# Performance work log

Measured on AMD Instinct MI355X. Metric: run time of the kernel, lower is better.

The kernel has to match this reference:

```python
import jax, jax.numpy as jnp
import numpy as np

LN_EPS = 1e-5

def _layernorm(x, g, b):
    m = jnp.mean(x, axis=-1, keepdims=True)
    v = jnp.var(x, axis=-1, keepdims=True)
    return (x - m) / jnp.sqrt(v + LN_EPS) * g + b

def setup_inputs() -> dict:
    key = jax.random.key(0)
    ks = jax.random.split(key, 16)
    N, E, D, P = 25000, 500000, 256, 64  # nodes, edges, node_dim, pair_dim
    def rn(k, shape, scale=1.0):
        return jax.random.normal(k, shape, dtype=jnp.float32) * scale
    return {
        "x": rn(ks[0], (N, D)),
        "rbf_r": rn(ks[1], (E, P)),
        "factor_r": jax.random.uniform(ks[2], (E, 1), dtype=jnp.float32),
        "sph_v0": rn(ks[3], (E, 5, 1)),  # l=2 spherical harmonics (5 comps)
        "sph_v1": rn(ks[4], (E, 3, 1)),  # l=1 spherical harmonics (3 comps)
        "W_down": rn(ks[5], (D, P), D ** -0.5),
        "b_down": jnp.zeros((P,), jnp.float32),
        "W_up0": rn(ks[6], (P, 2 * P), P ** -0.5),
        "b_up0": jnp.zeros((2 * P,), jnp.float32),
        "W_up1": rn(ks[7], (P, 2 * P), P ** -0.5),
        "W_uph": rn(ks[8], (P, 2 * P), P ** -0.5),
        "W_n1": rn(ks[9], (6 * P, D), (6 * P) ** -0.5),
        "b_n1": jnp.zeros((D,), jnp.float32),
        "ln_g": jnp.ones((D,), jnp.float32),
        "ln_b": jnp.zeros((D,), jnp.float32),
        "W_n2": rn(ks[10], (D, D), D ** -0.5),
        "b_n2": jnp.zeros((D,), jnp.float32),
        "j": jax.random.randint(ks[11], (E,), 0, N, dtype=jnp.int32),
        "i": jax.random.randint(ks[12], (E,), 0, N, dtype=jnp.int32),
    }

def reference(x, rbf_r, factor_r, sph_v0, sph_v1, W_down, b_down, W_up0, b_up0,
              W_up1, W_uph, W_n1, b_n1, ln_g, ln_b, W_n2, b_n2, j, i):
    N = x.shape[0]
    _x = x @ W_down + b_down                      # [N, P]
    l0_pair = _x[j] * rbf_r * factor_r            # [E, P]
    agg0 = jax.ops.segment_sum(l0_pair, i, num_segments=N)                     # [N, P]
    agg1 = jax.ops.segment_sum(l0_pair[:, None, :] * sph_v1, i, num_segments=N)  # [N, 3, P]
    aggh = jax.ops.segment_sum(l0_pair[:, None, :] * sph_v0, i, num_segments=N)  # [N, 5, P]
    l0_node = (_x * agg0) @ W_up0 + b_up0                                      # [N, 2P]
    l1_node = jnp.sum(jnp.square((_x[:, None, :] * agg1) @ W_up1), axis=1)     # [N, 2P]
    lh_node = jnp.sum(jnp.square((_x[:, None, :] * aggh) @ W_uph), axis=1)     # [N, 2P]
    node = jnp.concatenate([l0_node, l1_node, lh_node], axis=-1)               # [N, 6P]
    h = jax.nn.silu(_layernorm(node @ W_n1 + b_n1, ln_g, ln_b))
    return h @ W_n2 + b_n2 + x  # dropout is identity in eval
```

## Files before the change

### kernel.cpp

```cpp
#include <hip/hip_runtime.h>
#include <hip/hip_bf16.h>

typedef __attribute__((ext_vector_type(8))) short bf16x8;
typedef __attribute__((ext_vector_type(4))) float f32x4;

__device__ __forceinline__ unsigned short f2bf(float f) {
    unsigned u = __float_as_uint(f);
    return (unsigned short)((u + 0x7FFF + ((u >> 16) & 1)) >> 16);
}
__device__ __forceinline__ unsigned pack2(float a, float b) {
    return (unsigned)f2bf(a) | ((unsigned)f2bf(b) << 16);
}
__device__ __forceinline__ float ubf(unsigned short h) {
    return __uint_as_float((unsigned)h << 16);
}
__device__ __forceinline__ int RLi(float v, int k) {
    return __builtin_amdgcn_readlane(__float_as_int(v), k);
}
__device__ __forceinline__ float RLf(float v, int k) {
    return __uint_as_float((unsigned)__builtin_amdgcn_readlane(__float_as_int(v), k));
}

__device__ void swz_body(const float* __restrict__ W,
                         unsigned short* __restrict__ Bsw, int K, int idx)
{
    int total = (K >> 5) * 1024;
    if (idx >= total) return;
    int lane = idx & 63;
    int ct = (idx >> 6) & 15;
    int ks = idx >> 10;
    int col = ct * 16 + (lane & 15);
    int kbase = (ks << 5) + ((lane >> 4) << 3);
    const float* p = &W[(size_t)kbase * 256 + col];
    uint4 o;
    o.x = pack2(p[0 * 256], p[1 * 256]);
    o.y = pack2(p[2 * 256], p[3 * 256]);
    o.z = pack2(p[4 * 256], p[5 * 256]);
    o.w = pack2(p[6 * 256], p[7 * 256]);
    *(uint4*)&Bsw[(size_t)idx * 8] = o;
}

__device__ void swz_split_body(const float* __restrict__ W,
                               unsigned short* __restrict__ Bh,
                               unsigned short* __restrict__ Bl,
                               int K, int C, int idx)
{
    int ct_n = C >> 4;
    int total = (K >> 5) * ct_n * 64;
    if (idx >= total) return;
    int per_ks = ct_n * 64;
    int ks = idx / per_ks;
    int rem = idx - ks * per_ks;
    int ct = rem >> 6;
    int lane = rem & 63;
    int col = ct * 16 + (lane & 15);
    int kbase = (ks << 5) + ((lane >> 4) << 3);
    const float* p = &W[(size_t)kbase * C + col];
    unsigned short hs[8], ls[8];
#pragma unroll
    for (int j = 0; j < 8; j++) {
        float wv = p[(size_t)j * C];
        unsigned short h = f2bf(wv);
        hs[j] = h;
        ls[j] = f2bf(wv - ubf(h));
    }
    uint4 oh, ol;
    oh.x = (unsigned)hs[0] | ((unsigned)hs[1] << 16);
    oh.y = (unsigned)hs[2] | ((unsigned)hs[3] << 16);
    oh.z = (unsigned)hs[4] | ((unsigned)hs[5] << 16);
    oh.w = (unsigned)hs[6] | ((unsigned)hs[7] << 16);
    ol.x = (unsigned)ls[0] | ((unsigned)ls[1] << 16);
    ol.y = (unsigned)ls[2] | ((unsigned)ls[3] << 16);
    ol.z = (unsigned)ls[4] | ((unsigned)ls[5] << 16);
    ol.w = (unsigned)ls[6] | ((unsigned)ls[7] << 16);
    *(uint4*)&Bh[(size_t)idx * 8] = oh;
    *(uint4*)&Bl[(size_t)idx * 8] = ol;
}

__global__ __launch_bounds__(256) void k_prep(
    const float* __restrict__ Wn1, unsigned short* __restrict__ Bsw1,
    const float* __restrict__ Wn2, unsigned short* __restrict__ Bsw2,
    const float* __restrict__ Wu0, unsigned short* __restrict__ Wu0h, unsigned short* __restrict__ Wu0l,
    const float* __restrict__ Wu1, unsigned short* __restrict__ Wu1h, unsigned short* __restrict__ Wu1l,
    const float* __restrict__ Wuh, unsigned short* __restrict__ Wuhh, unsigned short* __restrict__ Wuhl,
    const float* __restrict__ Wd, unsigned short* __restrict__ Wdh, unsigned short* __restrict__ Wdl,
    int* __restrict__ counts, int N)
{
    int b = blockIdx.x;
    int tid = threadIdx.x;
    if (b < 48)       swz_body(Wn1, Bsw1, 384, b * 256 + tid);
    else if (b < 80)  swz_body(Wn2, Bsw2, 256, (b - 48) * 256 + tid);
    else if (b < 84)  swz_split_body(Wu0, Wu0h, Wu0l, 64, 128, (b - 80) * 256 + tid);
    else if (b < 88)  swz_split_body(Wu1, Wu1h, Wu1l, 64, 128, (b - 84) * 256 + tid);
    else if (b < 92)  swz_split_body(Wuh, Wuhh, Wuhl, 64, 128, (b - 88) * 256 + tid);
    else if (b < 100) swz_split_body(Wd, Wdh, Wdl, 256, 64, (b - 92) * 256 + tid);
    else {
        for (int i = (b - 100) * 256 + tid; i < N + 1; i += 25 * 256)
            counts[i] = 0;
    }
}

__global__ __launch_bounds__(256, 4) void k_down_hist(
    const float* __restrict__ x, const unsigned short* __restrict__ Wdh,
    const unsigned short* __restrict__ Wdl, const float* __restrict__ bd,
    float* __restrict__ xp, const int* __restrict__ iidx,
    int* __restrict__ counts, int N, int E, int nDown)
{
    __shared__ __align__(16) unsigned short Ahi[32 * 264];
    __shared__ __align__(16) unsigned short Alo[32 * 264];

    if ((int)blockIdx.x >= nDown) {
        int e = ((int)blockIdx.x - nDown) * 256 + threadIdx.x;
        if (e < E) atomicAdd(&counts[iidx[e]], 1);
        return;
    }

    int n0 = blockIdx.x * 32;
    int tid = threadIdx.x;
    int lane = tid & 63;
    int w = tid >> 6;
    int rt = w & 1;
    int cg = w >> 1;
    int lcol = lane & 15;
    int quad = lane >> 4;
    int kq = quad * 8;

    for (int t = tid; t < 32 * 64; t += 256) {
        int r = t >> 6, c4 = t & 63;
        int n = n0 + r;
        float4 v = {0.f, 0.f, 0.f, 0.f};
        if (n < N) v = *(const float4*)&x[(size_t)n * 256 + c4 * 4];
        unsigned short hx = f2bf(v.x), hy = f2bf(v.y);
        unsigned short hz = f2bf(v.z), hw = f2bf(v.w);
        uint2 oh, ol;
        oh.x = (unsigned)hx | ((unsigned)hy << 16);
        oh.y = (unsigned)hz | ((unsigned)hw << 16);
        ol.x = (unsigned)f2bf(v.x - ubf(hx)) | ((unsigned)f2bf(v.y - ubf(hy)) << 16);
        ol.y = (unsigned)f2bf(v.z - ubf(hz)) | ((unsigned)f2bf(v.w - ubf(hw)) << 16);
        *(uint2*)&Ahi[r * 264 + c4 * 4] = oh;
        *(uint2*)&Alo[r * 264 + c4 * 4] = ol;
    }
    __syncthreads();

    int arow = rt * 16 + lcol;
    f32x4 acc[2];
    acc[0] = (f32x4){0.f, 0.f, 0.f, 0.f};
    acc[1] = (f32x4){0.f, 0.f, 0.f, 0.f};
#pragma unroll
    for (int ks = 0; ks < 8; ks++) {
        bf16x8 ah = *(const bf16x8*)&Ahi[arow * 264 + ks * 32 + kq];
        bf16x8 al = *(const bf16x8*)&Alo[arow * 264 + ks * 32 + kq];
#pragma unroll
        for (int t = 0; t < 2; t++) {
            int ct = cg * 2 + t;
            size_t bi = ((size_t)((ks * 4 + ct) * 64 + lane)) * 8;
            bf16x8 bh = *(const bf16x8*)&Wdh[bi];
            bf16x8 bl = *(const bf16x8*)&Wdl[bi];
            acc[t] = __builtin_amdgcn_mfma_f32_16x16x32_bf16(ah, bh, acc[t], 0, 0, 0);
            acc[t] = __builtin_amdgcn_mfma_f32_16x16x32_bf16(ah, bl, acc[t], 0, 0, 0);
            acc[t] = __builtin_amdgcn_mfma_f32_16x16x32_bf16(al, bh, acc[t], 0, 0, 0);
        }
    }
#pragma unroll
    for (int t = 0; t < 2; t++) {
        int col = cg * 32 + t * 16 + lcol;
        float bb = bd[col];
#pragma unroll
        for (int q = 0; q < 4; q++) {
            int row = rt * 16 + quad * 4 + q;
            int n = n0 + row;
            if (n < N) xp[(size_t)n * 64 + col] = acc[t][q] + bb;
        }
    }
}

__global__ __launch_bounds__(1024) void k_scan(
    const int* __restrict__ counts, int* __restrict__ rowptr,
    int* __restrict__ cursor, int N)
{
    __shared__ int part[1024];
    int t = threadIdx.x;
    int chunk = (N + 1023) / 1024;
    int beg = t * chunk;
    int end = min(beg + chunk, N);
    int s = 0;
    for (int i = beg; i < end; i++) s += counts[i];
    part[t] = s;
    __syncthreads();
    for (int off = 1; off < 1024; off <<= 1) {
        int v = (t >= off) ? part[t - off] : 0;
        __syncthreads();
        part[t] += v;
        __syncthreads();
    }
    int run = (t == 0) ? 0 : part[t - 1];
    for (int i = beg; i < end; i++) {
        rowptr[i] = run;
        cursor[i] = run;
        run += counts[i];
    }
    if (t == 1023) rowptr[N] = part[1023];
}

__global__ __launch_bounds__(256) void k_scatter_pack(
    const int* __restrict__ iidx, const int* __restrict__ jidx,
    const float* __restrict__ factor, const float* __restrict__ sph0,
    const float* __restrict__ sph1, int* __restrict__ cursor,
    float* __restrict__ packed, int E)
{
    int e = blockIdx.x * 256 + threadIdx.x;
    if (e >= E) return;
    int pos = atomicAdd(&cursor[iidx[e]], 1);
    float4 w0, w1, w2;
    w0.x = __int_as_float(e);
    w0.y = __int_as_float(jidx[e]);
    w0.z = factor[e];
    w0.w = sph1[e * 3 + 0];
    w1.x = sph1[e * 3 + 1];
    w1.y = sph1[e * 3 + 2];
    w1.z = sph0[e * 5 + 0];
    w1.w = sph0[e * 5 + 1];
    w2.x = sph0[e * 5 + 2];
    w2.y = sph0[e * 5 + 3];
    w2.z = sph0[e * 5 + 4];
    w2.w = 0.f;
    float4* q = (float4*)&packed[(size_t)pos * 12];
    q[0] = w0; q[1] = w1; q[2] = w2;
}

__global__ __launch_bounds__(256) void k_gather(
    const float* __restrict__ xp, const float* __restrict__ rbf,
    const float* __restrict__ packed, const int* __restrict__ rowptr,
    unsigned short* __restrict__ aggHi, unsigned short* __restrict__ aggLo,
    int N)
{
    int n = blockIdx.x * 4 + (threadIdx.x >> 6);
    if (n >= N) return;
    int p = threadIdx.x & 63;
    int beg = rowptr[n], end = rowptr[n + 1];

    float a0 = 0.f;
    float a1x = 0.f, a1y = 0.f, a1z = 0.f;
    float h0 = 0.f, h1 = 0.f, h2 = 0.f, h3 = 0.f, h4 = 0.f;

    for (int base = beg; base < end; base += 64) {
        int m = end - base;
        if (m > 64) m = 64;
        float4 w0 = {0.f, 0.f, 0.f, 0.f};
        float4 w1 = {0.f, 0.f, 0.f, 0.f};
        float4 w2 = {0.f, 0.f, 0.f, 0.f};
        if (base + p < end) {
            const float4* q = (const float4*)&packed[(size_t)(base + p) * 12];
            w0 = q[0]; w1 = q[1]; w2 = q[2];
        }
        int k = 0;
        for (; k + 7 < m; k += 8) {
            int e0 = RLi(w0.x, k),     e1 = RLi(w0.x, k + 1);
            int e2 = RLi(w0.x, k + 2), e3 = RLi(w0.x, k + 3);
            int e4 = RLi(w0.x, k + 4), e5 = RLi(w0.x, k + 5);
            int e6 = RLi(w0.x, k + 6), e7 = RLi(w0.x, k + 7);
            int j0 = RLi(w0.y, k),     j1 = RLi(w0.y, k + 1);
            int j2 = RLi(w0.y, k + 2), j3 = RLi(w0.y, k + 3);
            int j4 = RLi(w0.y, k + 4), j5 = RLi(w0.y, k + 5);
            int j6 = RLi(w0.y, k + 6), j7 = RLi(w0.y, k + 7);
            float x0 = xp[(size_t)j0 * 64 + p], r0 = rbf[(size_t)e0 * 64 + p];
            float x1 = xp[(size_t)j1 * 64 + p], r1 = rbf[(size_t)e1 * 64 + p];
            float x2 = xp[(size_t)j2 * 64 + p], r2 = rbf[(size_t)e2 * 64 + p];
            float x3 = xp[(size_t)j3 * 64 + p], r3 = rbf[(size_t)e3 * 64 + p];
            float x4 = xp[(size_t)j4 * 64 + p], r4 = rbf[(size_t)e4 * 64 + p];
            float x5 = xp[(size_t)j5 * 64 + p], r5 = rbf[(size_t)e5 * 64 + p];
            float x6 = xp[(size_t)j6 * 64 + p], r6 = rbf[(size_t)e6 * 64 + p];
            float x7 = xp[(size_t)j7 * 64 + p], r7 = rbf[(size_t)e7 * 64 + p];
            float f0 = RLf(w0.z, k),     f1 = RLf(w0.z, k + 1);
            float f2 = RLf(w0.z, k + 2), f3 = RLf(w0.z, k + 3);
            float f4 = RLf(w0.z, k + 4), f5 = RLf(w0.z, k + 5);
            float f6 = RLf(w0.z, k + 6), f7 = RLf(w0.z, k + 7);
            float v0 = x0 * r0 * f0, v1 = x1 * r1 * f1;
            float v2 = x2 * r2 * f2, v3 = x3 * r3 * f3;
            float v4 = x4 * r4 * f4, v5 = x5 * r5 * f5;
            float v6 = x6 * r6 * f6, v7 = x7 * r7 * f7;
            a0 += ((v0 + v1) + (v2 + v3)) + ((v4 + v5) + (v6 + v7));
            a1x += ((v0 * RLf(w0.w, k)     + v1 * RLf(w0.w, k + 1))
                  + (v2 * RLf(w0.w, k + 2) + v3 * RLf(w0.w, k + 3)))
                 + ((v4 * RLf(w0.w, k + 4) + v5 * RLf(w0.w, k + 5))
                  + (v6 * RLf(w0.w, k + 6) + v7 * RLf(w0.w, k + 7)));
            a1y += ((v0 * RLf(w1.x, k)     + v1 * RLf(w1.x, k + 1))
                  + (v2 * RLf(w1.x, k + 2) + v3 * RLf(w1.x, k + 3)))
                 + ((v4 * RLf(w1.x, k + 4) + v5 * RLf(w1.x, k + 5))
                  + (v6 * RLf(w1.x, k + 6) + v7 * RLf(w1.x, k + 7)));
            a1z += ((v0 * RLf(w1.y, k)     + v1 * RLf(w1.y, k + 1))
                  + (v2 * RLf(w1.y, k + 2) + v3 * RLf(w1.y, k + 3)))
                 + ((v4 * RLf(w1.y, k + 4) + v5 * RLf(w1.y, k + 5))
                  + (v6 * RLf(w1.y, k + 6) + v7 * RLf(w1.y, k + 7)));
            h0  += ((v0 * RLf(w1.z, k)     + v1 * RLf(w1.z, k + 1))
                  + (v2 * RLf(w1.z, k + 2) + v3 * RLf(w1.z, k + 3)))
                 + ((v4 * RLf(w1.z, k + 4) + v5 * RLf(w1.z, k + 5))
                  + (v6 * RLf(w1.z, k + 6) + v7 * RLf(w1.z, k + 7)));
            h1  += ((v0 * RLf(w1.w, k)     + v1 * RLf(w1.w, k + 1))
                  + (v2 * RLf(w1.w, k + 2) + v3 * RLf(w1.w, k + 3)))
                 + ((v4 * RLf(w1.w, k + 4) + v5 * RLf(w1.w, k + 5))
                  + (v6 * RLf(w1.w, k + 6) + v7 * RLf(w1.w, k + 7)));
            h2  += ((v0 * RLf(w2.x, k)     + v1 * RLf(w2.x, k + 1))
                  + (v2 * RLf(w2.x, k + 2) + v3 * RLf(w2.x, k + 3)))
                 + ((v4 * RLf(w2.x, k + 4) + v5 * RLf(w2.x, k + 5))
                  + (v6 * RLf(w2.x, k + 6) + v7 * RLf(w2.x, k + 7)));
            h3  += ((v0 * RLf(w2.y, k)     + v1 * RLf(w2.y, k + 1))
                  + (v2 * RLf(w2.y, k + 2) + v3 * RLf(w2.y, k + 3)))
                 + ((v4 * RLf(w2.y, k + 4) + v5 * RLf(w2.y, k + 5))
                  + (v6 * RLf(w2.y, k + 6) + v7 * RLf(w2.y, k + 7)));
            h4  += ((v0 * RLf(w2.z, k)     + v1 * RLf(w2.z, k + 1))
                  + (v2 * RLf(w2.z, k + 2) + v3 * RLf(w2.z, k + 3)))
                 + ((v4 * RLf(w2.z, k + 4) + v5 * RLf(w2.z, k + 5))
                  + (v6 * RLf(w2.z, k + 6) + v7 * RLf(w2.z, k + 7)));
        }
        for (; k + 3 < m; k += 4) {
            int e0 = RLi(w0.x, k),     e1 = RLi(w0.x, k + 1);
            int e2 = RLi(w0.x, k + 2), e3 = RLi(w0.x, k + 3);
            int j0 = RLi(w0.y, k),     j1 = RLi(w0.y, k + 1);
            int j2 = RLi(w0.y, k + 2), j3 = RLi(w0.y, k + 3);
            float x0 = xp[(size_t)j0 * 64 + p], r0 = rbf[(size_t)e0 * 64 + p];
            float x1 = xp[(size_t)j1 * 64 + p], r1 = rbf[(size_t)e1 * 64 + p];
            float x2 = xp[(size_t)j2 * 64 + p], r2 = rbf[(size_t)e2 * 64 + p];
            float x3 = xp[(size_t)j3 * 64 + p], r3 = rbf[(size_t)e3 * 64 + p];
            float f0 = RLf(w0.z, k),     f1 = RLf(w0.z, k + 1);
            float f2 = RLf(w0.z, k + 2), f3 = RLf(w0.z, k + 3);
            float v0 = x0 * r0 * f0, v1 = x1 * r1 * f1;
            float v2 = x2 * r2 * f2, v3 = x3 * r3 * f3;
            a0 += (v0 + v1) + (v2 + v3);
            a1x += v0 * RLf(w0.w, k)     + v1 * RLf(w0.w, k + 1)
                 + v2 * RLf(w0.w, k + 2) + v3 * RLf(w0.w, k + 3);
            a1y += v0 * RLf(w1.x, k)     + v1 * RLf(w1.x, k + 1)
                 + v2 * RLf(w1.x, k + 2) + v3 * RLf(w1.x, k + 3);
            a1z += v0 * RLf(w1.y, k)     + v1 * RLf(w1.y, k + 1)
                 + v2 * RLf(w1.y, k + 2) + v3 * RLf(w1.y, k + 3);
            h0  += v0 * RLf(w1.z, k)     + v1 * RLf(w1.z, k + 1)
                 + v2 * RLf(w1.z, k + 2) + v3 * RLf(w1.z, k + 3);
            h1  += v0 * RLf(w1.w, k)     + v1 * RLf(w1.w, k + 1)
                 + v2 * RLf(w1.w, k + 2) + v3 * RLf(w1.w, k + 3);
            h2  += v0 * RLf(w2.x, k)     + v1 * RLf(w2.x, k + 1)
                 + v2 * RLf(w2.x, k + 2) + v3 * RLf(w2.x, k + 3);
            h3  += v0 * RLf(w2.y, k)     + v1 * RLf(w2.y, k + 1)
                 + v2 * RLf(w2.y, k + 2) + v3 * RLf(w2.y, k + 3);
            h4  += v0 * RLf(w2.z, k)     + v1 * RLf(w2.z, k + 1)
                 + v2 * RLf(w2.z, k + 2) + v3 * RLf(w2.z, k + 3);
        }
        for (; k < m; k++) {
            int e0 = RLi(w0.x, k);
            int j0 = RLi(w0.y, k);
            float f0 = RLf(w0.z, k);
            float v0 = xp[(size_t)j0 * 64 + p] * rbf[(size_t)e0 * 64 + p] * f0;
            a0 += v0;
            a1x += v0 * RLf(w0.w, k);
            a1y += v0 * RLf(w1.x, k);
            a1z += v0 * RLf(w1.y, k);
            h0  += v0 * RLf(w1.z, k);
            h1  += v0 * RLf(w1.w, k);
            h2  += v0 * RLf(w2.x, k);
            h3  += v0 * RLf(w2.y, k);
            h4  += v0 * RLf(w2.z, k);
        }
    }

    float xv = xp[(size_t)n * 64 + p];
    float vals[9] = {xv * a0, xv * a1x, xv * a1y, xv * a1z,
                     xv * h0, xv * h1, xv * h2, xv * h3, xv * h4};
    size_t b9 = (size_t)(n >> 4) * 9216 + (size_t)(n & 15) * 64 + p;
#pragma unroll
    for (int m = 0; m < 9; m++) {
        unsigned short hh = f2bf(vals[m]);
        aggHi[b9 + m * 1024] = hh;
        aggLo[b9 + m * 1024] = f2bf(vals[m] - ubf(hh));
    }
}

__global__ __launch_bounds__(256, 3) void k_node(
    const unsigned short* __restrict__ aggHi, const unsigned short* __restrict__ aggLo,
    const unsigned short* __restrict__ Wu0h, const unsigned short* __restrict__ Wu0l,
    const unsigned short* __restrict__ Wu1h, const unsigned short* __restrict__ Wu1l,
    const unsigned short* __restrict__ Wuhh, const unsigned short* __restrict__ Wuhl,
    const float* __restrict__ bu0, unsigned short* __restrict__ node, int N)
{
    __shared__ __align__(16) unsigned short Ahi[9 * 16 * 72];
    __shared__ __align__(16) unsigned short Alo[9 * 16 * 72];

    int n0 = blockIdx.x * 16;
    int tid = threadIdx.x;
    int lane = tid & 63;
    int w = tid >> 6;
    int lcol = lane & 15;
    int quad = lane >> 4;
    int kq = quad * 8;

    size_t gbase = (size_t)blockIdx.x * 9216;
    for (int t = tid; t < 1152; t += 256) {
        int row = t >> 3, c8 = t & 7;
        int n = n0 + (row & 15);
        uint4 v = {0u, 0u, 0u, 0u};
        if (n < N) v = *(const uint4*)&aggHi[gbase + (size_t)row * 64 + c8 * 8];
        *(uint4*)&Ahi[row * 72 + c8 * 8] = v;
    }
    for (int t = tid; t < 1152; t += 256) {
        int row = t >> 3, c8 = t & 7;
        int n = n0 + (row & 15);
        uint4 v = {0u, 0u, 0u, 0u};
        if (n < N) v = *(const uint4*)&aggLo[gbase + (size_t)row * 64 + c8 * 8];
        *(uint4*)&Alo[row * 72 + c8 * 8] = v;
    }
    __syncthreads();

    {
        bf16x8 bh[2][2], bl[2][2];
#pragma unroll
        for (int ks = 0; ks < 2; ks++)
#pragma unroll
            for (int t = 0; t < 2; t++) {
                size_t bi = ((size_t)((ks * 8 + w * 2 + t) * 64 + lane)) * 8;
                bh[ks][t] = *(const bf16x8*)&Wu0h[bi];
                bl[ks][t] = *(const bf16x8*)&Wu0l[bi];
            }
        f32x4 acc[2];
        acc[0] = (f32x4){0.f, 0.f, 0.f, 0.f};
        acc[1] = (f32x4){0.f, 0.f, 0.f, 0.f};
#pragma unroll
        for (int ks = 0; ks < 2; ks++) {
            bf16x8 ah = *(const bf16x8*)&Ahi[lcol * 72 + ks * 32 + kq];
            bf16x8 al = *(const bf16x8*)&Alo[lcol * 72 + ks * 32 + kq];
#pragma unroll
            for (int t = 0; t < 2; t++) {
                acc[t] = __builtin_amdgcn_mfma_f32_16x16x32_bf16(ah, bh[ks][t], acc[t], 0, 0, 0);
                acc[t] = __builtin_amdgcn_mfma_f32_16x16x32_bf16(ah, bl[ks][t], acc[t], 0, 0, 0);
                acc[t] = __builtin_amdgcn_mfma_f32_16x16x32_bf16(al, bh[ks][t], acc[t], 0, 0, 0);
            }
        }
#pragma unroll
        for (int t = 0; t < 2; t++) {
            int col = w * 32 + t * 16 + lcol;
            float bb = bu0[col];
#pragma unroll
            for (int q = 0; q < 4; q++) {
                int n = n0 + quad * 4 + q;
                if (n < N) node[(size_t)n * 384 + col] = f2bf(acc[t][q] + bb);
            }
        }
    }

    {
        bf16x8 bh[2][2], bl[2][2];
#pragma unroll
        for (int ks = 0; ks < 2; ks++)
#pragma unroll
            for (int t = 0; t < 2; t++) {
                size_t bi = ((size_t)((ks * 8 + w * 2 + t) * 64 + lane)) * 8;
                bh[ks][t] = *(const bf16x8*)&Wu1h[bi];
                bl[ks][t] = *(const bf16x8*)&Wu1l[bi];
            }
        f32x4 S[2];
        S[0] = (f32x4){0.f, 0.f, 0.f, 0.f};
        S[1] = (f32x4){0.f, 0.f, 0.f, 0.f};
#pragma unroll
        for (int c = 0; c < 3; c++) {
            f32x4 d[2];
            d[0] = (f32x4){0.f, 0.f, 0.f, 0.f};
            d[1] = (f32x4){0.f, 0.f, 0.f, 0.f};
            int abase = (1 + c) * (16 * 72);
#pragma unroll
            for (int ks = 0; ks < 2; ks++) {
                bf16x8 ah = *(const bf16x8*)&Ahi[abase + lcol * 72 + ks * 32 + kq];
                bf16x8 al = *(const bf16x8*)&Alo[abase + lcol * 72 + ks * 32 + kq];
#pragma unroll
                for (int t = 0; t < 2; t++) {
                    d[t] = __builtin_amdgcn_mfma_f32_16x16x32_bf16(ah, bh[ks][t], d[t], 0, 0, 0);
                    d[t] = __builtin_amdgcn_mfma_f32_16x16x32_bf16(ah, bl[ks][t], d[t], 0, 0, 0);
                    d[t] = __builtin_amdgcn_mfma_f32_16x16x32_bf16(al, bh[ks][t], d[t], 0, 0, 0);
                }
            }
            S[0] += d[0] * d[0];
            S[1] += d[1] * d[1];
        }
#pragma unroll
        for (int t = 0; t < 2; t++) {
            int col = w * 32 + t * 16 + lcol;
#pragma unroll
            for (int q = 0; q < 4; q++) {
                int n = n0 + quad * 4 + q;
                if (n < N) node[(size_t)n * 384 + 128 + col] = f2bf(S[t][q]);
            }
        }
    }

    {
        bf16x8 bh[2][2], bl[2][2];
#pragma unroll
        for (int ks = 0; ks < 2; ks++)
#pragma unroll
            for (int t = 0; t < 2; t++) {
                size_t bi = ((size_t)((ks * 8 + w * 2 + t) * 64 + lane)) * 8;
                bh[ks][t] = *(const bf16x8*)&Wuhh[bi];
                bl[ks][t] = *(const bf16x8*)&Wuhl[bi];
            }
        f32x4 S[2];
        S[0] = (f32x4){0.f, 0.f, 0.f, 0.f};
        S[1] = (f32x4){0.f, 0.f, 0.f, 0.f};
#pragma unroll
        for (int c = 0; c < 5; c++) {
            f32x4 d[2];
            d[0] = (f32x4){0.f, 0.f, 0.f, 0.f};
            d[1] = (f32x4){0.f, 0.f, 0.f, 0.f};
            int abase = (4 + c) * (16 * 72);
#pragma unroll
            for (int ks = 0; ks < 2; ks++) {
                bf16x8 ah = *(const bf16x8*)&Ahi[abase + lcol * 72 + ks * 32 + kq];
                bf16x8 al = *(const bf16x8*)&Alo[abase + lcol * 72 + ks * 32 + kq];
#pragma unroll
                for (int t = 0; t < 2; t++) {
                    d[t] = __builtin_amdgcn_mfma_f32_16x16x32_bf16(ah, bh[ks][t], d[t], 0, 0, 0);
                    d[t] = __builtin_amdgcn_mfma_f32_16x16x32_bf16(ah, bl[ks][t], d[t], 0, 0, 0);
                    d[t] = __builtin_amdgcn_mfma_f32_16x16x32_bf16(al, bh[ks][t], d[t], 0, 0, 0);
                }
            }
            S[0] += d[0] * d[0];
            S[1] += d[1] * d[1];
        }
#pragma unroll
        for (int t = 0; t < 2; t++) {
            int col = w * 32 + t * 16 + lcol;
#pragma unroll
            for (int q = 0; q < 4; q++) {
                int n = n0 + quad * 4 + q;
                if (n < N) node[(size_t)n * 384 + 256 + col] = f2bf(S[t][q]);
            }
        }
    }
}

__global__ __launch_bounds__(256, 4) void k_final(
    const unsigned short* __restrict__ node, const unsigned short* __restrict__ Bsw1,
    const float* __restrict__ bn1, const float* __restrict__ lng,
    const float* __restrict__ lnb, const unsigned short* __restrict__ Bsw2,
    const float* __restrict__ bn2, const float* __restrict__ x,
    float* __restrict__ out, int N)
{
    __shared__ __align__(16) unsigned short Abf[32 * 392];
    __shared__ float red[32][33];
    __shared__ float red2[32][33];
    __shared__ float mstat[32][2];

    int n0 = blockIdx.x * 32;
    int tid = threadIdx.x;
    int lane = tid & 63;
    int w = tid >> 6;
    int rt = w & 1;
    int cg = w >> 1;
    int lcol = lane & 15;
    int quad = lane >> 4;
    int arow = rt * 16 + lcol;
    int kq = quad * 8;

    for (int i = tid; i < 32 * 48; i += 256) {
        int r = i / 48, c8 = i - r * 48;
        int n = n0 + r;
        uint4 v = {0u, 0u, 0u, 0u};
        if (n < N) v = *(const uint4*)&node[(size_t)n * 384 + c8 * 8];
        *(uint4*)&Abf[r * 392 + c8 * 8] = v;
    }
    __syncthreads();

    f32x4 acc[8];
#pragma unroll
    for (int t = 0; t < 8; t++) acc[t] = (f32x4){0.f, 0.f, 0.f, 0.f};
    for (int ks = 0; ks < 12; ks++) {
        bf16x8 a = *(const bf16x8*)&Abf[arow * 392 + ks * 32 + kq];
        const bf16x8* bp =
            (const bf16x8*)&Bsw1[(size_t)(((ks * 16 + cg * 8) * 64) + lane) * 8];
#pragma unroll
        for (int t = 0; t < 8; t++)
            acc[t] = __builtin_amdgcn_mfma_f32_16x16x32_bf16(a, bp[t * 64], acc[t], 0, 0, 0);
    }

    float bias[8];
#pragma unroll
    for (int t = 0; t < 8; t++) bias[t] = bn1[cg * 128 + t * 16 + lcol];
#pragma unroll
    for (int q = 0; q < 4; q++) {
        float s = 0.f, s2 = 0.f;
#pragma unroll
        for (int t = 0; t < 8; t++) {
            float v = acc[t][q] + bias[t];
            s += v; s2 += v * v;
        }
        int row = rt * 16 + quad * 4 + q;
        red[row][cg * 16 + lcol] = s;
        red2[row][cg * 16 + lcol] = s2;
    }
    __syncthreads();
    {
        int row = tid >> 3, g = tid & 7;
        float s = 0.f, s2 = 0.f;
#pragma unroll
        for (int u = 0; u < 4; u++) {
            s  += red[row][g * 4 + u];
            s2 += red2[row][g * 4 + u];
        }
        s  += __shfl_down(s, 4);  s2 += __shfl_down(s2, 4);
        s  += __shfl_down(s, 2);  s2 += __shfl_down(s2, 2);
        s  += __shfl_down(s, 1);  s2 += __shfl_down(s2, 1);
        if (g == 0) {
            float mn = s * (1.f / 256.f);
            float var = s2 * (1.f / 256.f) - mn * mn;
            mstat[row][0] = mn;
            mstat[row][1] = rsqrtf(var + 1e-5f);
        }
    }
    __syncthreads();

#pragma unroll
    for (int t = 0; t < 8; t++) {
        int col = cg * 128 + t * 16 + lcol;
        float gg = lng[col], bb = lnb[col];
#pragma unroll
        for (int q = 0; q < 4; q++) {
            int row = rt * 16 + quad * 4 + q;
            float z = (acc[t][q] + bias[t] - mstat[row][0]) * mstat[row][1] * gg + bb;
            float h = z / (1.f + __expf(-z));
            Abf[row * 264 + col] = f2bf(h);
        }
    }
    __syncthreads();

    f32x4 o[8];
#pragma unroll
    for (int t = 0; t < 8; t++) o[t] = (f32x4){0.f, 0.f, 0.f, 0.f};
    for (int ks = 0; ks < 8; ks++) {
        bf16x8 a = *(const bf16x8*)&Abf[arow * 264 + ks * 32 + kq];
        const bf16x8* bp =
            (const bf16x8*)&Bsw2[(size_t)(((ks * 16 + cg * 8) * 64) + lane) * 8];
#pragma unroll
        for (int t = 0; t < 8; t++)
            o[t] = __builtin_amdgcn_mfma_f32_16x16x32_bf16(a, bp[t * 64], o[t], 0, 0, 0);
    }
#pragma unroll
    for (int t = 0; t < 8; t++) {
        int col = cg * 128 + t * 16 + lcol;
        float ob = bn2[col];
#pragma unroll
        for (int q = 0; q < 4; q++) {
            int row = rt * 16 + quad * 4 + q;
            int n = n0 + row;
            if (n < N)
                out[(size_t)n * 256 + col] = o[t][q] + ob + x[(size_t)n * 256 + col];
        }
    }
}

extern "C" void kernel_launch(void* const* d_in, const int* in_sizes, int n_in,
                              void* d_out, int out_size, void* d_ws, size_t ws_size,
                              hipStream_t stream)
{
    const float* x      = (const float*)d_in[0];
    const float* rbf    = (const float*)d_in[1];
    const float* factor = (const float*)d_in[2];
    const float* sph0   = (const float*)d_in[3];
    const float* sph1   = (const float*)d_in[4];
    const float* Wd     = (const float*)d_in[5];
    const float* bd     = (const float*)d_in[6];
    const float* Wu0    = (const float*)d_in[7];
    const float* bu0    = (const float*)d_in[8];
    const float* Wu1    = (const float*)d_in[9];
    const float* Wuh    = (const float*)d_in[10];
    const float* Wn1    = (const float*)d_in[11];
    const float* bn1    = (const float*)d_in[12];
    const float* lng    = (const float*)d_in[13];
    const float* lnb    = (const float*)d_in[14];
    const float* Wn2    = (const float*)d_in[15];
    const float* bn2    = (const float*)d_in[16];
    const int*   jidx   = (const int*)d_in[17];
    const int*   iidx   = (const int*)d_in[18];
    float* out = (float*)d_out;

    int N = in_sizes[0] / 256;
    int E = in_sizes[17];
    int nblk = (N + 15) / 16;

    float* ws   = (float*)d_ws;
    float* xp   = ws;
    float* aggF = xp + (size_t)N * 64;
    unsigned short* aggHi = (unsigned short*)aggF;
    unsigned short* aggLo = aggHi + (size_t)nblk * 9216;
    float* nodeF = aggF + (size_t)nblk * 9216;
    unsigned short* nodeB = (unsigned short*)nodeF;
    unsigned short* Bsw1 = (unsigned short*)(nodeF + (size_t)N * 384);
    unsigned short* Bsw2 = Bsw1 + 12 * 16 * 64 * 8;
    unsigned short* Wu0h_s = Bsw2 + 8 * 16 * 64 * 8;
    unsigned short* Wu0l_s = Wu0h_s + 64 * 128;
    unsigned short* Wu1h_s = Wu0l_s + 64 * 128;
    unsigned short* Wu1l_s = Wu1h_s + 64 * 128;
    unsigned short* Wuhh_s = Wu1l_s + 64 * 128;
    unsigned short* Wuhl_s = Wuhh_s + 64 * 128;
    unsigned short* Wdh_s  = Wuhl_s + 64 * 128;
    unsigned short* Wdl_s  = Wdh_s + 256 * 64;

    int* counts  = (int*)nodeF;
    int* rowptr  = counts + (N + 1);
    int* cursor  = rowptr + (N + 1);
    float* packed = nodeF + 131072;

    int nDown = (N + 31) / 32;
    int nHist = (E + 255) / 256;

    k_prep<<<dim3(125), dim3(256), 0, stream>>>(
        Wn1, Bsw1, Wn2, Bsw2, Wu0, Wu0h_s, Wu0l_s, Wu1, Wu1h_s, Wu1l_s,
        Wuh, Wuhh_s, Wuhl_s, Wd, Wdh_s, Wdl_s, counts, N);
    k_down_hist<<<dim3(nDown + nHist), dim3(256), 0, stream>>>(
        x, Wdh_s, Wdl_s, bd, xp, iidx, counts, N, E, nDown);
    k_scan<<<dim3(1), dim3(1024), 0, stream>>>(counts, rowptr, cursor, N);
    k_scatter_pack<<<dim3(nHist), dim3(256), 0, stream>>>(
        iidx, jidx, factor, sph0, sph1, cursor, packed, E);
    k_gather<<<dim3((N + 3) / 4), dim3(256), 0, stream>>>(
        xp, rbf, packed, rowptr, aggHi, aggLo, N);
    k_node<<<dim3(nblk), dim3(256), 0, stream>>>(
        aggHi, aggLo, Wu0h_s, Wu0l_s, Wu1h_s, Wu1l_s, Wuhh_s, Wuhl_s,
        bu0, nodeB, N);
    k_final<<<dim3((N + 31) / 32), dim3(256), 0, stream>>>(
        nodeB, Bsw1, bn1, lng, lnb, Bsw2, bn2, x, out, N);
}
```

Measured before the change: 448.1 us.

## Store down-projected features as bf16 and fuse down GEMM with scatter-pack

Result: no change. 445.8 us (-0.5%).

```diff
diff --git a/kernel.cpp b/kernel.cpp
--- a/kernel.cpp
+++ b/kernel.cpp
@@ -100,18 +100,73 @@
     }
 }
 
-__global__ __launch_bounds__(256, 4) void k_down_hist(
+__global__ __launch_bounds__(256) void k_hist(
+    const int* __restrict__ iidx, int* __restrict__ counts, int E)
+{
+    int e = blockIdx.x * 256 + threadIdx.x;
+    if (e < E) atomicAdd(&counts[iidx[e]], 1);
+}
+
+__global__ __launch_bounds__(1024) void k_scan(
+    const int* __restrict__ counts, int* __restrict__ rowptr,
+    int* __restrict__ cursor, int N)
+{
+    __shared__ int part[1024];
+    int t = threadIdx.x;
+    int chunk = (N + 1023) / 1024;
+    int beg = t * chunk;
+    int end = min(beg + chunk, N);
+    int s = 0;
+    for (int i = beg; i < end; i++) s += counts[i];
+    part[t] = s;
+    __syncthreads();
+    for (int off = 1; off < 1024; off <<= 1) {
+        int v = (t >= off) ? part[t - off] : 0;
+        __syncthreads();
+        part[t] += v;
+        __syncthreads();
+    }
+    int run = (t == 0) ? 0 : part[t - 1];
+    for (int i = beg; i < end; i++) {
+        rowptr[i] = run;
+        cursor[i] = run;
+        run += counts[i];
+    }
+    if (t == 1023) rowptr[N] = part[1023];
+}
+
+__global__ __launch_bounds__(256, 4) void k_down_scatter(
     const float* __restrict__ x, const unsigned short* __restrict__ Wdh,
     const unsigned short* __restrict__ Wdl, const float* __restrict__ bd,
-    float* __restrict__ xp, const int* __restrict__ iidx,
-    int* __restrict__ counts, int N, int E, int nDown)
+    unsigned short* __restrict__ xpB,
+    const int* __restrict__ iidx, const int* __restrict__ jidx,
+    const float* __restrict__ factor, const float* __restrict__ sph0,
+    const float* __restrict__ sph1, int* __restrict__ cursor,
+    float* __restrict__ packed, int N, int E, int nDown)
 {
     __shared__ __align__(16) unsigned short Ahi[32 * 264];
     __shared__ __align__(16) unsigned short Alo[32 * 264];
 
     if ((int)blockIdx.x >= nDown) {
         int e = ((int)blockIdx.x - nDown) * 256 + threadIdx.x;
-        if (e < E) atomicAdd(&counts[iidx[e]], 1);
+        if (e < E) {
+            int pos = atomicAdd(&cursor[iidx[e]], 1);
+            float4 w0, w1, w2;
+            w0.x = __int_as_float(e);
+            w0.y = __int_as_float(jidx[e]);
+            w0.z = factor[e];
+            w0.w = sph1[e * 3 + 0];
+            w1.x = sph1[e * 3 + 1];
+            w1.y = sph1[e * 3 + 2];
+            w1.z = sph0[e * 5 + 0];
+            w1.w = sph0[e * 5 + 1];
+            w2.x = sph0[e * 5 + 2];
+            w2.y = sph0[e * 5 + 3];
+            w2.z = sph0[e * 5 + 4];
+            w2.w = 0.f;
+            float4* q = (float4*)&packed[(size_t)pos * 12];
+            q[0] = w0; q[1] = w1; q[2] = w2;
+        }
         return;
     }
 
@@ -169,67 +224,13 @@
         for (int q = 0; q < 4; q++) {
             int row = rt * 16 + quad * 4 + q;
             int n = n0 + row;
-            if (n < N) xp[(size_t)n * 64 + col] = acc[t][q] + bb;
-        }
-    }
-}
-
-__global__ __launch_bounds__(1024) void k_scan(
-    const int* __restrict__ counts, int* __restrict__ rowptr,
-    int* __restrict__ cursor, int N)
-{
-    __shared__ int part[1024];
-    int t = threadIdx.x;
-    int chunk = (N + 1023) / 1024;
-    int beg = t * chunk;
-    int end = min(beg + chunk, N);
-    int s = 0;
-    for (int i = beg; i < end; i++) s += counts[i];
-    part[t] = s;
-    __syncthreads();
-    for (int off = 1; off < 1024; off <<= 1) {
-        int v = (t >= off) ? part[t - off] : 0;
-        __syncthreads();
-        part[t] += v;
-        __syncthreads();
-    }
-    int run = (t == 0) ? 0 : part[t - 1];
-    for (int i = beg; i < end; i++) {
-        rowptr[i] = run;
-        cursor[i] = run;
-        run += counts[i];
-    }
-    if (t == 1023) rowptr[N] = part[1023];
-}
-
-__global__ __launch_bounds__(256) void k_scatter_pack(
-    const int* __restrict__ iidx, const int* __restrict__ jidx,
-    const float* __restrict__ factor, const float* __restrict__ sph0,
-    const float* __restrict__ sph1, int* __restrict__ cursor,
-    float* __restrict__ packed, int E)
-{
-    int e = blockIdx.x * 256 + threadIdx.x;
-    if (e >= E) return;
-    int pos = atomicAdd(&cursor[iidx[e]], 1);
-    float4 w0, w1, w2;
-    w0.x = __int_as_float(e);
-    w0.y = __int_as_float(jidx[e]);
-    w0.z = factor[e];
-    w0.w = sph1[e * 3 + 0];
-    w1.x = sph1[e * 3 + 1];
-    w1.y = sph1[e * 3 + 2];
-    w1.z = sph0[e * 5 + 0];
-    w1.w = sph0[e * 5 + 1];
-    w2.x = sph0[e * 5 + 2];
-    w2.y = sph0[e * 5 + 3];
-    w2.z = sph0[e * 5 + 4];
-    w2.w = 0.f;
-    float4* q = (float4*)&packed[(size_t)pos * 12];
-    q[0] = w0; q[1] = w1; q[2] = w2;
+            if (n < N) xpB[(size_t)n * 64 + col] = f2bf(acc[t][q] + bb);
+        }
+    }
 }
 
 __global__ __launch_bounds__(256) void k_gather(
-    const float* __restrict__ xp, const float* __restrict__ rbf,
+    const unsigned short* __restrict__ xpB, const float* __restrict__ rbf,
     const float* __restrict__ packed, const int* __restrict__ rowptr,
     unsigned short* __restrict__ aggHi, unsigned short* __restrict__ aggLo,
     int N)
@@ -263,14 +264,14 @@
             int j2 = RLi(w0.y, k + 2), j3 = RLi(w0.y, k + 3);
             int j4 = RLi(w0.y, k + 4), j5 = RLi(w0.y, k + 5);
             int j6 = RLi(w0.y, k + 6), j7 = RLi(w0.y, k + 7);
-            float x0 = xp[(size_t)j0 * 64 + p], r0 = rbf[(size_t)e0 * 64 + p];
-            float x1 = xp[(size_t)j1 * 64 + p], r1 = rbf[(size_t)e1 * 64 + p];
-            float x2 = xp[(size_t)j2 * 64 + p], r2 = rbf[(size_t)e2 * 64 + p];
-            float x3 = xp[(size_t)j3 * 64 + p], r3 = rbf[(size_t)e3 * 64 + p];
-            float x4 = xp[(size_t)j4 * 64 + p], r4 = rbf[(size_t)e4 * 64 + p];
-            float x5 = xp[(size_t)j5 * 64 + p], r5 = rbf[(size_t)e5 * 64 + p];
-            float x6 = xp[(size_t)j6 * 64 + p], r6 = rbf[(size_t)e6 * 64 + p];
-            float x7 = xp[(size_t)j7 * 64 + p], r7 = rbf[(size_t)e7 * 64 + p];
+            float x0 = ubf(xpB[(size_t)j0 * 64 + p]), r0 = rbf[(size_t)e0 * 64 + p];
+            float x1 = ubf(xpB[(size_t)j1 * 64 + p]), r1 = rbf[(size_t)e1 * 64 + p];
+            float x2 = ubf(xpB[(size_t)j2 * 64 + p]), r2 = rbf[(size_t)e2 * 64 + p];
+            float x3 = ubf(xpB[(size_t)j3 * 64 + p]), r3 = rbf[(size_t)e3 * 64 + p];
+            float x4 = ubf(xpB[(size_t)j4 * 64 + p]), r4 = rbf[(size_t)e4 * 64 + p];
+            float x5 = ubf(xpB[(size_t)j5 * 64 + p]), r5 = rbf[(size_t)e5 * 64 + p];
+            float x6 = ubf(xpB[(size_t)j6 * 64 + p]), r6 = rbf[(size_t)e6 * 64 + p];
+            float x7 = ubf(xpB[(size_t)j7 * 64 + p]), r7 = rbf[(size_t)e7 * 64 + p];
             float f0 = RLf(w0.z, k),     f1 = RLf(w0.z, k + 1);
             float f2 = RLf(w0.z, k + 2), f3 = RLf(w0.z, k + 3);
             float f4 = RLf(w0.z, k + 4), f5 = RLf(w0.z, k + 5);
@@ -318,10 +319,10 @@
             int e2 = RLi(w0.x, k + 2), e3 = RLi(w0.x, k + 3);
             int j0 = RLi(w0.y, k),     j1 = RLi(w0.y, k + 1);
             int j2 = RLi(w0.y, k + 2), j3 = RLi(w0.y, k + 3);
-            float x0 = xp[(size_t)j0 * 64 + p], r0 = rbf[(size_t)e0 * 64 + p];
-            float x1 = xp[(size_t)j1 * 64 + p], r1 = rbf[(size_t)e1 * 64 + p];
-            float x2 = xp[(size_t)j2 * 64 + p], r2 = rbf[(size_t)e2 * 64 + p];
-            float x3 = xp[(size_t)j3 * 64 + p], r3 = rbf[(size_t)e3 * 64 + p];
+            float x0 = ubf(xpB[(size_t)j0 * 64 + p]), r0 = rbf[(size_t)e0 * 64 + p];
+            float x1 = ubf(xpB[(size_t)j1 * 64 + p]), r1 = rbf[(size_t)e1 * 64 + p];
+            float x2 = ubf(xpB[(size_t)j2 * 64 + p]), r2 = rbf[(size_t)e2 * 64 + p];
+            float x3 = ubf(xpB[(size_t)j3 * 64 + p]), r3 = rbf[(size_t)e3 * 64 + p];
             float f0 = RLf(w0.z, k),     f1 = RLf(w0.z, k + 1);
             float f2 = RLf(w0.z, k + 2), f3 = RLf(w0.z, k + 3);
             float v0 = x0 * r0 * f0, v1 = x1 * r1 * f1;
@@ -348,7 +349,7 @@
             int e0 = RLi(w0.x, k);
             int j0 = RLi(w0.y, k);
             float f0 = RLf(w0.z, k);
-            float v0 = xp[(size_t)j0 * 64 + p] * rbf[(size_t)e0 * 64 + p] * f0;
+            float v0 = ubf(xpB[(size_t)j0 * 64 + p]) * rbf[(size_t)e0 * 64 + p] * f0;
             a0 += v0;
             a1x += v0 * RLf(w0.w, k);
             a1y += v0 * RLf(w1.x, k);
@@ -361,7 +362,7 @@
         }
     }
 
-    float xv = xp[(size_t)n * 64 + p];
+    float xv = ubf(xpB[(size_t)n * 64 + p]);
     float vals[9] = {xv * a0, xv * a1x, xv * a1y, xv * a1z,
                      xv * h0, xv * h1, xv * h2, xv * h3, xv * h4};
     size_t b9 = (size_t)(n >> 4) * 9216 + (size_t)(n & 15) * 64 + p;
@@ -682,8 +683,8 @@
     int nblk = (N + 15) / 16;
 
     float* ws   = (float*)d_ws;
-    float* xp   = ws;
-    float* aggF = xp + (size_t)N * 64;
+    unsigned short* xpB = (unsigned short*)ws;
+    float* aggF = ws + (size_t)N * 32;
     unsigned short* aggHi = (unsigned short*)aggF;
     unsigned short* aggLo = aggHi + (size_t)nblk * 9216;
     float* nodeF = aggF + (size_t)nblk * 9216;
@@ -705,18 +706,18 @@
     float* packed = nodeF + 131072;
 
     int nDown = (N + 31) / 32;
-    int nHist = (E + 255) / 256;
+    int nScat = (E + 255) / 256;
 
     k_prep<<<dim3(125), dim3(256), 0, stream>>>(
         Wn1, Bsw1, Wn2, Bsw2, Wu0, Wu0h_s, Wu0l_s, Wu1, Wu1h_s, Wu1l_s,
         Wuh, Wuhh_s, Wuhl_s, Wd, Wdh_s, Wdl_s, counts, N);
-    k_down_hist<<<dim3(nDown + nHist), dim3(256), 0, stream>>>(
-        x, Wdh_s, Wdl_s, bd, xp, iidx, counts, N, E, nDown);
+    k_hist<<<dim3(nScat), dim3(256), 0, stream>>>(iidx, counts, E);
     k_scan<<<dim3(1), dim3(1024), 0, stream>>>(counts, rowptr, cursor, N);
-    k_scatter_pack<<<dim3(nHist), dim3(256), 0, stream>>>(
-        iidx, jidx, factor, sph0, sph1, cursor, packed, E);
+    k_down_scatter<<<dim3(nDown + nScat), dim3(256), 0, stream>>>(
+        x, Wdh_s, Wdl_s, bd, xpB, iidx, jidx, factor, sph0, sph1,
+        cursor, packed, N, E, nDown);
     k_gather<<<dim3((N + 3) / 4), dim3(256), 0, stream>>>(
-        xp, rbf, packed, rowptr, aggHi, aggLo, N);
+        xpB, rbf, packed, rowptr, aggHi, aggLo, N);
     k_node<<<dim3(nblk), dim3(256), 0, stream>>>(
         aggHi, aggLo, Wu0h_s, Wu0l_s, Wu1h_s, Wu1l_s, Wuhh_s, Wuhl_s,
         bu0, nodeB, N);
```
